# Kernel tuning notes

Measured on AMD Instinct MI355X. Metric: run time of the kernel, lower is better.

## Reference

```python
import jax, jax.numpy as jnp
import numpy as np

NS = 150  # MC weight samples


def setup_inputs() -> dict:
    key = jax.random.key(0)
    mu_shapes = {
        'mu_W0': (512, 784), 'mu_b0': (512,),
        'mu_W1': (512, 512), 'mu_b1': (512,),
        'mu_W2': (512, 512), 'mu_b2': (512,),
        'mu_W3': (10, 512),  'mu_b3': (10,),
    }
    ks = list(jax.random.split(key, 2 * len(mu_shapes) + 1))
    inp = {'x': jax.random.normal(ks[0], (64, 784), jnp.float32)}
    i = 1
    for name, shp in mu_shapes.items():
        inp[name] = jax.random.normal(ks[i], shp, jnp.float32) * 0.05
        i += 1
    for name, shp in mu_shapes.items():
        # log-std around -3 => std ~ 0.05
        inp['v_' + name[3:]] = jax.random.normal(ks[i], shp, jnp.float32) * 0.1 - 3.0
        i += 1
    return inp


def _sample(k, mu, v):
    # original: r = randn_like(m) * sqrt(exp(2*v)) == randn * exp(v); param = r + m
    eps = jax.random.normal(k, (NS,) + mu.shape, mu.dtype)
    return mu + jnp.exp(v) * eps  # [NS, *mu.shape]


def reference(x, mu_W0, mu_b0, mu_W1, mu_b1, mu_W2, mu_b2, mu_W3, mu_b3,
              v_W0, v_b0, v_W1, v_b1, v_W2, v_b2, v_W3, v_b3):
    ks = jax.random.split(jax.random.key(1), 8)
    W0 = _sample(ks[0], mu_W0, v_W0); b0 = _sample(ks[1], mu_b0, v_b0)
    W1 = _sample(ks[2], mu_W1, v_W1); b1 = _sample(ks[3], mu_b1, v_b1)
    W2 = _sample(ks[4], mu_W2, v_W2); b2 = _sample(ks[5], mu_b2, v_b2)
    W3 = _sample(ks[6], mu_W3, v_W3); b3 = _sample(ks[7], mu_b3, v_b3)
    # batched-over-samples MLP forward: s = sample, b = batch
    h = jax.nn.relu(jnp.einsum('bi,soi->sbo', x, W0) + b0[:, None, :])
    h = jax.nn.relu(jnp.einsum('sbi,soi->sbo', h, W1) + b1[:, None, :])
    h = jax.nn.relu(jnp.einsum('sbi,soi->sbo', h, W2) + b2[:, None, :])
    out = jnp.einsum('sbi,soi->sbo', h, W3) + b3[:, None, :]  # [NS, B, 10]
    return out
```

## Files before the change

kernel.cpp:

```cpp
#include <hip/hip_runtime.h>


typedef short bf16x8 __attribute__((ext_vector_type(8)));
typedef int   i32x4  __attribute__((ext_vector_type(4)));
typedef float f32x4  __attribute__((ext_vector_type(4)));

#define TF_R(r) { x0 += x1; x1 = (x1 << (r)) | (x1 >> (32 - (r))); x1 ^= x0; }

#define TF8(r) { _Pragma("unroll") for (int j = 0; j < 8; ++j) { \
    a[j] += b[j]; b[j] = (b[j] << (r)) | (b[j] >> (32 - (r))); b[j] ^= a[j]; } }
#define INJ8(kka, kkb) { _Pragma("unroll") for (int j = 0; j < 8; ++j) { \
    a[j] += (kka); b[j] += (kkb); } }

__device__ __forceinline__ unsigned int tf_xor(unsigned int k0, unsigned int k1,
                                               unsigned int c1)
{
  const unsigned int ks2 = k0 ^ k1 ^ 0x1BD11BDAu;
  unsigned int x0 = k0;
  unsigned int x1 = c1 + k1;
  TF_R(13) TF_R(15) TF_R(26) TF_R(6)
  x0 += k1;  x1 += ks2 + 1u;
  TF_R(17) TF_R(29) TF_R(16) TF_R(24)
  x0 += ks2; x1 += k0 + 2u;
  TF_R(13) TF_R(15) TF_R(26) TF_R(6)
  x0 += k0;  x1 += k1 + 3u;
  TF_R(17) TF_R(29) TF_R(16) TF_R(24)
  x0 += k1;  x1 += ks2 + 4u;
  TF_R(13) TF_R(15) TF_R(26) TF_R(6)
  x0 += ks2; x1 += k0 + 5u;
  return x0 ^ x1;
}

__device__ __forceinline__ float bits_to_g(unsigned int r)
{
  float f = __uint_as_float((r >> 9) | 0x3F800000u) - 1.0f;
  float x = __builtin_fmaf(f, 2.0f, -0.99999994f);
  float L = __log2f(__builtin_fmaf(-x, x, 1.0f));
  float t  = __builtin_fmaf(L, -0.6931472f, -2.5f);
  float pc = -4.39150654e-06f;
  pc = __builtin_fmaf(pc, t, 0.00021858087f);
  pc = __builtin_fmaf(pc, t, -0.00125372503f);
  pc = __builtin_fmaf(pc, t, -0.00417768164f);
  pc = __builtin_fmaf(pc, t, 0.246640727f);
  pc = __builtin_fmaf(pc, t, 1.50140941f);
  float w  = L * -0.6931472f;
  float t2 = sqrtf(w) - 3.0f;
  float pt = 0.00573950773f;
  pt = __builtin_fmaf(pt, t2, -0.0076224613f);
  pt = __builtin_fmaf(pt, t2, 0.00943887047f);
  pt = __builtin_fmaf(pt, t2, 1.00167406f);
  pt = __builtin_fmaf(pt, t2, 2.83297682f);
  float p = (L > -7.2134752f) ? pc : pt;
  return p * x;
}

__device__ __forceinline__ unsigned short f32_to_bf16_rne(float v)
{
  unsigned int u = __float_as_uint(v);
  unsigned int r = (u + 0x7FFFu + ((u >> 16) & 1u)) >> 16;
  return (unsigned short)r;
}

__device__ __forceinline__ unsigned int pack_bf16_rne(float a, float b)
{
  unsigned int ua = __float_as_uint(a);
  unsigned int ub = __float_as_uint(b);
  ua += 0x7FFFu + ((ua >> 16) & 1u);
  ub += 0x7FFFu + ((ub >> 16) & 1u);
  return __builtin_amdgcn_perm(ub, ua, 0x07060302u);
}

__global__ __launch_bounds__(256) void xpad_kernel(const float* __restrict__ x,
                                                   unsigned short* __restrict__ xp)
{
  int i = blockIdx.x * 256 + threadIdx.x;
  if (i >= 64 * 832) return;
  int m = i / 832, k = i - m * 832;
  float v = (k < 784) ? x[m * 784 + k] : 0.0f;
  xp[i] = f32_to_bf16_rne(v);
}

__global__ __launch_bounds__(256) void pack_kernel(
    const float* __restrict__ muW0, const float* __restrict__ vW0,
    const float* __restrict__ muW1, const float* __restrict__ vW1,
    const float* __restrict__ muW2, const float* __restrict__ vW2,
    const float* __restrict__ muW3, const float* __restrict__ vW3,
    float2* __restrict__ msP0, float2* __restrict__ msP1,
    float2* __restrict__ msP2, float2* __restrict__ msP3)
{
  int b = blockIdx.x, tid = threadIdx.x;
  const float* mu; const float* v; float2* o;
  int KV, NV, osh, base;
  if (b < 1664)      { mu = muW0; v = vW0; o = msP0; KV = 784; NV = 512; osh = 9; base = 0;    }
  else if (b < 2688) { mu = muW1; v = vW1; o = msP1; KV = 512; NV = 512; osh = 9; base = 1664; }
  else if (b < 3712) { mu = muW2; v = vW2; o = msP2; KV = 512; NV = 512; osh = 9; base = 2688; }
  else               { mu = muW3; v = vW3; o = msP3; KV = 512; NV = 10;  osh = 4; base = 3712; }
  int e = (b - base) * 256 + tid;
  int k = (e & 7) | ((e >> (3 + osh)) << 3);
  int n = (e >> 3) & ((1 << osh) - 1);
  float2 r = {0.0f, 0.0f};
  if (k < KV && n < NV) {
    r.x = mu[n * KV + k];
    r.y = __expf(v[n * KV + k]) * 1.41421356237f;
  }
  o[e] = r;
}

__global__ __launch_bounds__(256) void bias_kernel(
    const float* __restrict__ mu0, const float* __restrict__ v0, float* __restrict__ o0,
    const float* __restrict__ mu1, const float* __restrict__ v1, float* __restrict__ o1,
    const float* __restrict__ mu2, const float* __restrict__ v2, float* __restrict__ o2,
    const float* __restrict__ mu3, const float* __restrict__ v3, float* __restrict__ o3,
    unsigned int k00, unsigned int k01, unsigned int k10, unsigned int k11,
    unsigned int k20, unsigned int k21, unsigned int k30, unsigned int k31)
{
  int b = blockIdx.x, tid = threadIdx.x;
  int seg = b / 300; if (seg > 3) seg = 3;
  const float* mu; const float* v; float* o; unsigned int ka, kb; int n;
  if      (seg == 0) { mu = mu0; v = v0; o = o0; ka = k00; kb = k01; n = 76800; }
  else if (seg == 1) { mu = mu1; v = v1; o = o1; ka = k10; kb = k11; n = 76800; }
  else if (seg == 2) { mu = mu2; v = v2; o = o2; ka = k20; kb = k21; n = 76800; }
  else               { mu = mu3; v = v3; o = o3; ka = k30; kb = k31; n = 1500;  }
  int e = (b - seg * 300) * 256 + tid;
  if (e >= n) return;
  int oo = (seg == 3) ? (e % 10) : (e & 511);
  float eps = 1.41421356237f * bits_to_g(tf_xor(ka, kb, (unsigned int)e));
  o[e] = __builtin_fmaf(__expf(v[oo]), eps, mu[oo]);
}

template<int KVALID, int KPAD, int OVALID, int OPITCH, int ASTRIDE, int AROW,
         bool RELU, bool F32OUT>
__global__
__attribute__((amdgpu_flat_work_group_size(256, 256)))
__attribute__((amdgpu_waves_per_eu(1, 4)))
void layer_fused(
    const unsigned short* __restrict__ A,
    void* __restrict__ OutV,
    const float2* __restrict__ msP,
    const float* __restrict__ bS,
    unsigned int k0, unsigned int k1)
{
  constexpr int NSTEPS = KPAD / 32;
  const unsigned int ks2 = k0 ^ k1 ^ 0x1BD11BDAu;
  const int s    = blockIdx.y;
  const int tid  = threadIdx.x;
  const int wave = tid >> 6, lane = tid & 63;
  const int quad = lane >> 4;
  const int n16  = lane & 15;
  const int nlane = blockIdx.x * 16 + n16;

  const unsigned short* As = A + (size_t)s * ASTRIDE;
  const unsigned int idx_base = (unsigned int)s * (unsigned int)(OVALID * KVALID)
                              + (unsigned int)nlane * (unsigned int)KVALID;

  f32x4 acc[4] = {f32x4{0,0,0,0}, f32x4{0,0,0,0}, f32x4{0,0,0,0}, f32x4{0,0,0,0}};

  auto load_step = [&](int st, bf16x8 (&af)[4], float4 (&q)[4]) {
    const int kb = st * 32 + quad * 8;
    #pragma unroll
    for (int mt = 0; mt < 4; ++mt)
      af[mt] = *reinterpret_cast<const bf16x8*>(
          As + (size_t)(mt * 16 + n16) * AROW + kb);
    const float4* mp = reinterpret_cast<const float4*>(
        msP + ((size_t)(kb >> 3) * OPITCH + nlane) * 8);
    #pragma unroll
    for (int h = 0; h < 4; ++h)
      q[h] = mp[h];
  };

  auto compute_step = [&](int st, bf16x8 (&af)[4], float4 (&q)[4]) {
    const int kb = st * 32 + quad * 8;

    unsigned int a[8], b[8];
    const unsigned int cb = idx_base + (unsigned int)kb + k1;
    #pragma unroll
    for (int j = 0; j < 8; ++j) { a[j] = k0; b[j] = cb + (unsigned int)j; }
    TF8(13) TF8(15) TF8(26) TF8(6)  INJ8(k1, ks2 + 1u)
    TF8(17) TF8(29) TF8(16) TF8(24) INJ8(ks2, k0 + 2u)
    TF8(13) TF8(15) TF8(26) TF8(6)  INJ8(k0, k1 + 3u)
    TF8(17) TF8(29) TF8(16) TF8(24) INJ8(k1, ks2 + 4u)
    TF8(13) TF8(15) TF8(26) TF8(6)  INJ8(ks2, k0 + 5u)

    float g[8];
    #pragma unroll
    for (int j = 0; j < 8; ++j)
      g[j] = bits_to_g(a[j] ^ b[j]);

    float wv[8];
    wv[0] = __builtin_fmaf(q[0].y, g[0], q[0].x);
    wv[1] = __builtin_fmaf(q[0].w, g[1], q[0].z);
    wv[2] = __builtin_fmaf(q[1].y, g[2], q[1].x);
    wv[3] = __builtin_fmaf(q[1].w, g[3], q[1].z);
    wv[4] = __builtin_fmaf(q[2].y, g[4], q[2].x);
    wv[5] = __builtin_fmaf(q[2].w, g[5], q[2].z);
    wv[6] = __builtin_fmaf(q[3].y, g[6], q[3].x);
    wv[7] = __builtin_fmaf(q[3].w, g[7], q[3].z);

    i32x4 bp;
    #pragma unroll
    for (int h = 0; h < 4; ++h)
      bp[h] = (int)pack_bf16_rne(wv[2 * h], wv[2 * h + 1]);
    bf16x8 bfrag = __builtin_bit_cast(bf16x8, bp);

    #pragma unroll
    for (int mt = 0; mt < 4; ++mt)
      acc[mt] = __builtin_amdgcn_mfma_f32_16x16x32_bf16(af[mt], bfrag, acc[mt], 0, 0, 0);
  };

  bf16x8 afA[4], afB[4];
  float4 qA[4], qB[4];
  int st = wave;
  if (st < NSTEPS) load_step(st, afA, qA);
  while (st < NSTEPS) {
    int n1 = st + 4;
    if (n1 < NSTEPS) load_step(n1, afB, qB);
    __builtin_amdgcn_sched_barrier(0);
    compute_step(st, afA, qA);
    st = n1;
    if (st >= NSTEPS) break;
    int n2 = st + 4;
    if (n2 < NSTEPS) load_step(n2, afA, qA);
    __builtin_amdgcn_sched_barrier(0);
    compute_step(st, afB, qB);
    st = n2;
  }

  __shared__ float red[4 * 16 * 64];
  #pragma unroll
  for (int mt = 0; mt < 4; ++mt)
    #pragma unroll
    for (int r = 0; r < 4; ++r)
      red[(wave * 16 + mt * 4 + r) * 64 + lane] = acc[mt][r];
  __syncthreads();

  const int m   = tid >> 2;
  const int nq  = (tid & 3) * 4;
  const int row = (m >> 4) * 4 + (m & 3);
  const int col = ((m >> 2) & 3) * 16 + nq;

  float4 p0 = *reinterpret_cast<const float4*>(&red[(0 * 16 + row) * 64 + col]);
  float4 p1 = *reinterpret_cast<const float4*>(&red[(1 * 16 + row) * 64 + col]);
  float4 p2 = *reinterpret_cast<const float4*>(&red[(2 * 16 + row) * 64 + col]);
  float4 p3 = *reinterpret_cast<const float4*>(&red[(3 * 16 + row) * 64 + col]);
  float v0 = (p0.x + p1.x) + (p2.x + p3.x);
  float v1 = (p0.y + p1.y) + (p2.y + p3.y);
  float v2 = (p0.z + p1.z) + (p2.z + p3.z);
  float v3 = (p0.w + p1.w) + (p2.w + p3.w);

  if (F32OUT) {
    float* Out = (float*)OutV;
    float vv[4] = {v0, v1, v2, v3};
    #pragma unroll
    for (int jj = 0; jj < 4; ++jj) {
      int nn = nq + jj;
      if (nn < OVALID)
        Out[((size_t)s * 64 + m) * OVALID + nn] = vv[jj] + bS[s * OVALID + nn];
    }
  } else {
    const float4 b4 = *reinterpret_cast<const float4*>(
        &bS[s * OVALID + blockIdx.x * 16 + nq]);
    float o0 = v0 + b4.x, o1 = v1 + b4.y, o2 = v2 + b4.z, o3 = v3 + b4.w;
    if (RELU) {
      o0 = fmaxf(o0, 0.0f); o1 = fmaxf(o1, 0.0f);
      o2 = fmaxf(o2, 0.0f); o3 = fmaxf(o3, 0.0f);
    }
    uint2 stv;
    stv.x = pack_bf16_rne(o0, o1);
    stv.y = pack_bf16_rne(o2, o3);
    *reinterpret_cast<uint2*>(
        (unsigned short*)OutV + ((size_t)s * 64 + m) * OPITCH + blockIdx.x * 16 + nq) = stv;
  }
}

static void tf_host(unsigned int k0, unsigned int k1, unsigned int c0, unsigned int c1,
                    unsigned int* o0, unsigned int* o1)
{
  const unsigned int ks2 = k0 ^ k1 ^ 0x1BD11BDAu;
  unsigned int x0 = c0 + k0, x1 = c1 + k1;
  TF_R(13) TF_R(15) TF_R(26) TF_R(6)
  x0 += k1;  x1 += ks2 + 1u;
  TF_R(17) TF_R(29) TF_R(16) TF_R(24)
  x0 += ks2; x1 += k0 + 2u;
  TF_R(13) TF_R(15) TF_R(26) TF_R(6)
  x0 += k0;  x1 += k1 + 3u;
  TF_R(17) TF_R(29) TF_R(16) TF_R(24)
  x0 += k1;  x1 += ks2 + 4u;
  TF_R(13) TF_R(15) TF_R(26) TF_R(6)
  x0 += ks2; x1 += k0 + 5u;
  *o0 = x0; *o1 = x1;
}

extern "C" void kernel_launch(void* const* d_in, const int* in_sizes, int n_in,
                              void* d_out, int out_size, void* d_ws, size_t ws_size,
                              hipStream_t stream)
{
  (void)in_sizes; (void)n_in; (void)out_size; (void)ws_size;

  const float* x    = (const float*)d_in[0];
  const float* muW0 = (const float*)d_in[1];
  const float* mub0 = (const float*)d_in[2];
  const float* muW1 = (const float*)d_in[3];
  const float* mub1 = (const float*)d_in[4];
  const float* muW2 = (const float*)d_in[5];
  const float* mub2 = (const float*)d_in[6];
  const float* muW3 = (const float*)d_in[7];
  const float* mub3 = (const float*)d_in[8];
  const float* vW0  = (const float*)d_in[9];
  const float* vb0  = (const float*)d_in[10];
  const float* vW1  = (const float*)d_in[11];
  const float* vb1  = (const float*)d_in[12];
  const float* vW2  = (const float*)d_in[13];
  const float* vb2  = (const float*)d_in[14];
  const float* vW3  = (const float*)d_in[15];
  const float* vb3  = (const float*)d_in[16];

  unsigned int key[8][2];
  for (unsigned int i = 0; i < 8; ++i)
    tf_host(0u, 1u, 0u, i, &key[i][0], &key[i][1]);

  char* ws = (char*)d_ws;
  unsigned short* xp = (unsigned short*)(ws);
  unsigned short* hA = (unsigned short*)(ws + 106496);
  float* b0s  = (float*)(ws + 9936896);
  float* b1s  = (float*)(ws + 10244096);
  float* b2s  = (float*)(ws + 10551296);
  float* b3s  = (float*)(ws + 10858496);
  float2* msP1 = (float2*)(ws + 10866688);
  float2* msP2 = (float2*)(ws + 12963840);
  float2* msP3 = (float2*)(ws + 15060992);
  float2* msP0 = (float2*)(ws + 15126528);
  unsigned short* hB = (unsigned short*)(ws + 15126528);

  xpad_kernel<<<208, 256, 0, stream>>>(x, xp);
  pack_kernel<<<3744, 256, 0, stream>>>(muW0, vW0, muW1, vW1, muW2, vW2, muW3, vW3,
                                        msP0, msP1, msP2, msP3);
  bias_kernel<<<906, 256, 0, stream>>>(mub0, vb0, b0s, mub1, vb1, b1s,
                                       mub2, vb2, b2s, mub3, vb3, b3s,
                                       key[1][0], key[1][1], key[3][0], key[3][1],
                                       key[5][0], key[5][1], key[7][0], key[7][1]);

  layer_fused<784, 832, 512, 512, 0,     832, true,  false>
      <<<dim3(32, 150), 256, 0, stream>>>(xp, hA, msP0, b0s, key[0][0], key[0][1]);
  layer_fused<512, 512, 512, 512, 32768, 512, true,  false>
      <<<dim3(32, 150), 256, 0, stream>>>(hA, hB, msP1, b1s, key[2][0], key[2][1]);
  layer_fused<512, 512, 512, 512, 32768, 512, true,  false>
      <<<dim3(32, 150), 256, 0, stream>>>(hB, hA, msP2, b2s, key[4][0], key[4][1]);
  layer_fused<512, 512, 10,  16,  32768, 512, false, true>
      <<<dim3(1, 150), 256, 0, stream>>>(hA, d_out, msP3, b3s, key[6][0], key[6][1]);
}
```

Baseline: 453.8 us.

## Split fused weight-sampling GEMM into separate weight-generation and GEMM kernels

```diff
diff --git a/kernel.cpp b/kernel.cpp
--- a/kernel.cpp
+++ b/kernel.cpp
@@ -128,6 +128,133 @@
   o[e] = __builtin_fmaf(__expf(v[oo]), eps, mu[oo]);
 }
 
+template<int KVALID, int KPAD>
+__global__ __launch_bounds__(256) void genw_kernel(
+    unsigned short* __restrict__ W,
+    const float2* __restrict__ msP,
+    unsigned int k0, unsigned int k1)
+{
+  constexpr int CPR = KPAD / 32;
+  const unsigned int ks2 = k0 ^ k1 ^ 0x1BD11BDAu;
+  const int e = blockIdx.x * 256 + threadIdx.x;
+  const int s = blockIdx.y;
+  const int n = e / CPR;
+  const int c32 = e - n * CPR;
+  const int k32 = c32 * 32;
+
+  const unsigned int cb0 = (unsigned int)s * (unsigned int)(512 * KVALID)
+                         + (unsigned int)n * (unsigned int)KVALID
+                         + (unsigned int)k32;
+  unsigned short* wp = W + ((size_t)(s * 512 + n) * KPAD + k32);
+
+  #pragma unroll
+  for (int h = 0; h < 4; ++h) {
+    const int kb = k32 + h * 8;
+    const float4* mp = reinterpret_cast<const float4*>(
+        msP + ((size_t)(kb >> 3) * 512 + n) * 8);
+    float4 q0 = mp[0], q1 = mp[1], q2 = mp[2], q3 = mp[3];
+
+    unsigned int a[8], b[8];
+    const unsigned int cb = cb0 + (unsigned int)(h * 8) + k1;
+    #pragma unroll
+    for (int j = 0; j < 8; ++j) { a[j] = k0; b[j] = cb + (unsigned int)j; }
+    TF8(13) TF8(15) TF8(26) TF8(6)  INJ8(k1, ks2 + 1u)
+    TF8(17) TF8(29) TF8(16) TF8(24) INJ8(ks2, k0 + 2u)
+    TF8(13) TF8(15) TF8(26) TF8(6)  INJ8(k0, k1 + 3u)
+    TF8(17) TF8(29) TF8(16) TF8(24) INJ8(k1, ks2 + 4u)
+    TF8(13) TF8(15) TF8(26) TF8(6)  INJ8(ks2, k0 + 5u)
+
+    float g[8];
+    #pragma unroll
+    for (int j = 0; j < 8; ++j)
+      g[j] = bits_to_g(a[j] ^ b[j]);
+
+    float wv[8];
+    wv[0] = __builtin_fmaf(q0.y, g[0], q0.x);
+    wv[1] = __builtin_fmaf(q0.w, g[1], q0.z);
+    wv[2] = __builtin_fmaf(q1.y, g[2], q1.x);
+    wv[3] = __builtin_fmaf(q1.w, g[3], q1.z);
+    wv[4] = __builtin_fmaf(q2.y, g[4], q2.x);
+    wv[5] = __builtin_fmaf(q2.w, g[5], q2.z);
+    wv[6] = __builtin_fmaf(q3.y, g[6], q3.x);
+    wv[7] = __builtin_fmaf(q3.w, g[7], q3.z);
+
+    i32x4 bp;
+    #pragma unroll
+    for (int hh = 0; hh < 4; ++hh)
+      bp[hh] = (int)pack_bf16_rne(wv[2 * hh], wv[2 * hh + 1]);
+    *reinterpret_cast<i32x4*>(wp + h * 8) = bp;
+  }
+}
+
+template<int KPAD, int ASTRIDE, int AROW>
+__global__ __launch_bounds__(256) void gemm_kernel(
+    const unsigned short* __restrict__ A,
+    unsigned short* __restrict__ Out,
+    const unsigned short* __restrict__ W,
+    const float* __restrict__ bS,
+    int unused0, int unused1)
+{
+  constexpr int NSTEPS = KPAD / 32;
+  const int s    = blockIdx.y;
+  const int tid  = threadIdx.x;
+  const int wave = tid >> 6, lane = tid & 63;
+  const int quad = lane >> 4;
+  const int n16  = lane & 15;
+  const int nlane = blockIdx.x * 16 + n16;
+
+  const unsigned short* As = A + (size_t)s * ASTRIDE;
+  const unsigned short* Wr = W + (size_t)(s * 512 + nlane) * KPAD;
+
+  f32x4 acc[4] = {f32x4{0,0,0,0}, f32x4{0,0,0,0}, f32x4{0,0,0,0}, f32x4{0,0,0,0}};
+
+  #pragma unroll 1
+  for (int st = wave; st < NSTEPS; st += 4) {
+    const int kb = st * 32 + quad * 8;
+    bf16x8 afrag[4];
+    #pragma unroll
+    for (int mt = 0; mt < 4; ++mt)
+      afrag[mt] = *reinterpret_cast<const bf16x8*>(
+          As + (size_t)(mt * 16 + n16) * AROW + kb);
+    bf16x8 bfrag = *reinterpret_cast<const bf16x8*>(Wr + kb);
+    #pragma unroll
+    for (int mt = 0; mt < 4; ++mt)
+      acc[mt] = __builtin_amdgcn_mfma_f32_16x16x32_bf16(afrag[mt], bfrag, acc[mt], 0, 0, 0);
+  }
+
+  __shared__ float red[4 * 16 * 64];
+  #pragma unroll
+  for (int mt = 0; mt < 4; ++mt)
+    #pragma unroll
+    for (int r = 0; r < 4; ++r)
+      red[(wave * 16 + mt * 4 + r) * 64 + lane] = acc[mt][r];
+  __syncthreads();
+
+  const int m   = tid >> 2;
+  const int nq  = (tid & 3) * 4;
+  const int row = (m >> 4) * 4 + (m & 3);
+  const int col = ((m >> 2) & 3) * 16 + nq;
+
+  float4 p0 = *reinterpret_cast<const float4*>(&red[(0 * 16 + row) * 64 + col]);
+  float4 p1 = *reinterpret_cast<const float4*>(&red[(1 * 16 + row) * 64 + col]);
+  float4 p2 = *reinterpret_cast<const float4*>(&red[(2 * 16 + row) * 64 + col]);
+  float4 p3 = *reinterpret_cast<const float4*>(&red[(3 * 16 + row) * 64 + col]);
+  float v0 = (p0.x + p1.x) + (p2.x + p3.x);
+  float v1 = (p0.y + p1.y) + (p2.y + p3.y);
+  float v2 = (p0.z + p1.z) + (p2.z + p3.z);
+  float v3 = (p0.w + p1.w) + (p2.w + p3.w);
+
+  const float4 b4 = *reinterpret_cast<const float4*>(
+      &bS[s * 512 + blockIdx.x * 16 + nq]);
+  float o0 = fmaxf(v0 + b4.x, 0.0f), o1 = fmaxf(v1 + b4.y, 0.0f);
+  float o2 = fmaxf(v2 + b4.z, 0.0f), o3 = fmaxf(v3 + b4.w, 0.0f);
+  uint2 stv;
+  stv.x = pack_bf16_rne(o0, o1);
+  stv.y = pack_bf16_rne(o2, o3);
+  *reinterpret_cast<uint2*>(
+      Out + ((size_t)s * 64 + m) * 512 + blockIdx.x * 16 + nq) = stv;
+}
+
 template<int KVALID, int KPAD, int OVALID, int OPITCH, int ASTRIDE, int AROW,
          bool RELU, bool F32OUT>
 __global__
@@ -170,7 +297,6 @@
 
   auto compute_step = [&](int st, bf16x8 (&af)[4], float4 (&q)[4]) {
     const int kb = st * 32 + quad * 8;
-
     unsigned int a[8], b[8];
     const unsigned int cb = idx_base + (unsigned int)kb + k1;
     #pragma unroll
@@ -294,7 +420,7 @@
                               void* d_out, int out_size, void* d_ws, size_t ws_size,
                               hipStream_t stream)
 {
-  (void)in_sizes; (void)n_in; (void)out_size; (void)ws_size;
+  (void)in_sizes; (void)n_in; (void)out_size;
 
   const float* x    = (const float*)d_in[0];
   const float* muW0 = (const float*)d_in[1];
@@ -330,6 +456,10 @@
   float2* msP3 = (float2*)(ws + 15060992);
   float2* msP0 = (float2*)(ws + 15126528);
   unsigned short* hB = (unsigned short*)(ws + 15126528);
+  unsigned short* Wbuf = (unsigned short*)(ws + 25165824);
+
+  const bool splitMid = ws_size >= (size_t)25165824 + 78643200u;
+  const bool splitL0  = ws_size >= (size_t)25165824 + 127795200u;
 
   xpad_kernel<<<208, 256, 0, stream>>>(x, xp);
   pack_kernel<<<3744, 256, 0, stream>>>(muW0, vW0, muW1, vW1, muW2, vW2, muW3, vW3,
@@ -339,12 +469,32 @@
                                        key[1][0], key[1][1], key[3][0], key[3][1],
                                        key[5][0], key[5][1], key[7][0], key[7][1]);
 
-  layer_fused<784, 832, 512, 512, 0,     832, true,  false>
-      <<<dim3(32, 150), 256, 0, stream>>>(xp, hA, msP0, b0s, key[0][0], key[0][1]);
-  layer_fused<512, 512, 512, 512, 32768, 512, true,  false>
-      <<<dim3(32, 150), 256, 0, stream>>>(hA, hB, msP1, b1s, key[2][0], key[2][1]);
-  layer_fused<512, 512, 512, 512, 32768, 512, true,  false>
-      <<<dim3(32, 150), 256, 0, stream>>>(hB, hA, msP2, b2s, key[4][0], key[4][1]);
-  layer_fused<512, 512, 10,  16,  32768, 512, false, true>
+  if (splitL0) {
+    genw_kernel<784, 832><<<dim3(52, 150), 256, 0, stream>>>(
+        Wbuf, msP0, key[0][0], key[0][1]);
+    gemm_kernel<832, 0, 832><<<dim3(32, 150), 256, 0, stream>>>(
+        xp, hA, Wbuf, b0s, 0, 0);
+  } else {
+    layer_fused<784, 832, 512, 512, 0, 832, true, false>
+        <<<dim3(32, 150), 256, 0, stream>>>(xp, hA, msP0, b0s, key[0][0], key[0][1]);
+  }
+
+  if (splitMid) {
+    genw_kernel<512, 512><<<dim3(32, 150), 256, 0, stream>>>(
+        Wbuf, msP1, key[2][0], key[2][1]);
+    gemm_kernel<512, 32768, 512><<<dim3(32, 150), 256, 0, stream>>>(
+        hA, hB, Wbuf, b1s, 0, 0);
+    genw_kernel<512, 512><<<dim3(32, 150), 256, 0, stream>>>(
+        Wbuf, msP2, key[4][0], key[4][1]);
+    gemm_kernel<512, 32768, 512><<<dim3(32, 150), 256, 0, stream>>>(
+        hB, hA, Wbuf, b2s, 0, 0);
+  } else {
+    layer_fused<512, 512, 512, 512, 32768, 512, true, false>
+        <<<dim3(32, 150), 256, 0, stream>>>(hA, hB, msP1, b1s, key[2][0], key[2][1]);
+    layer_fused<512, 512, 512, 512, 32768, 512, true, false>
+        <<<dim3(32, 150), 256, 0, stream>>>(hB, hA, msP2, b2s, key[4][0], key[4][1]);
+  }
+
+  layer_fused<512, 512, 10, 16, 32768, 512, false, true>
       <<<dim3(1, 150), 256, 0, stream>>>(hA, d_out, msP3, b3s, key[6][0], key[6][1]);
 }
```

Result: slower. 609.2 us (+34.2%).

## Split final layer across K with atomic accumulation and bias-prefilled output

Applied to the files above, without the earlier changes.

```diff
diff --git a/kernel.cpp b/kernel.cpp
--- a/kernel.cpp
+++ b/kernel.cpp
@@ -128,19 +128,30 @@
   o[e] = __builtin_fmaf(__expf(v[oo]), eps, mu[oo]);
 }
 
-template<int KVALID, int KPAD, int OVALID, int OPITCH, int ASTRIDE, int AROW,
-         bool RELU, bool F32OUT>
+__global__ __launch_bounds__(256) void bias3_out(float* __restrict__ Out,
+                                                 const float* __restrict__ b3s)
+{
+  int i = blockIdx.x * 256 + threadIdx.x;
+  if (i >= 96000) return;
+  int s = i / 640;
+  int rem = i - s * 640;
+  int n = rem % 10;
+  Out[i] = b3s[s * 10 + n];
+}
+
+template<int KVALID, int KPAD, int ASTRIDE, int AROW>
 __global__
 __attribute__((amdgpu_flat_work_group_size(256, 256)))
 __attribute__((amdgpu_waves_per_eu(1, 4)))
 void layer_fused(
     const unsigned short* __restrict__ A,
-    void* __restrict__ OutV,
+    unsigned short* __restrict__ Out,
     const float2* __restrict__ msP,
     const float* __restrict__ bS,
     unsigned int k0, unsigned int k1)
 {
   constexpr int NSTEPS = KPAD / 32;
+  constexpr int OVALID = 512, OPITCH = 512;
   const unsigned int ks2 = k0 ^ k1 ^ 0x1BD11BDAu;
   const int s    = blockIdx.y;
   const int tid  = threadIdx.x;
@@ -170,7 +181,6 @@
 
   auto compute_step = [&](int st, bf16x8 (&af)[4], float4 (&q)[4]) {
     const int kb = st * 32 + quad * 8;
-
     unsigned int a[8], b[8];
     const unsigned int cb = idx_base + (unsigned int)kb + k1;
     #pragma unroll
@@ -247,28 +257,106 @@
   float v2 = (p0.z + p1.z) + (p2.z + p3.z);
   float v3 = (p0.w + p1.w) + (p2.w + p3.w);
 
-  if (F32OUT) {
-    float* Out = (float*)OutV;
-    float vv[4] = {v0, v1, v2, v3};
-    #pragma unroll
-    for (int jj = 0; jj < 4; ++jj) {
-      int nn = nq + jj;
-      if (nn < OVALID)
-        Out[((size_t)s * 64 + m) * OVALID + nn] = vv[jj] + bS[s * OVALID + nn];
-    }
-  } else {
-    const float4 b4 = *reinterpret_cast<const float4*>(
-        &bS[s * OVALID + blockIdx.x * 16 + nq]);
-    float o0 = v0 + b4.x, o1 = v1 + b4.y, o2 = v2 + b4.z, o3 = v3 + b4.w;
-    if (RELU) {
-      o0 = fmaxf(o0, 0.0f); o1 = fmaxf(o1, 0.0f);
-      o2 = fmaxf(o2, 0.0f); o3 = fmaxf(o3, 0.0f);
-    }
-    uint2 stv;
-    stv.x = pack_bf16_rne(o0, o1);
-    stv.y = pack_bf16_rne(o2, o3);
-    *reinterpret_cast<uint2*>(
-        (unsigned short*)OutV + ((size_t)s * 64 + m) * OPITCH + blockIdx.x * 16 + nq) = stv;
+  const float4 b4 = *reinterpret_cast<const float4*>(
+      &bS[s * OVALID + blockIdx.x * 16 + nq]);
+  float o0 = fmaxf(v0 + b4.x, 0.0f), o1 = fmaxf(v1 + b4.y, 0.0f);
+  float o2 = fmaxf(v2 + b4.z, 0.0f), o3 = fmaxf(v3 + b4.w, 0.0f);
+  uint2 stv;
+  stv.x = pack_bf16_rne(o0, o1);
+  stv.y = pack_bf16_rne(o2, o3);
+  *reinterpret_cast<uint2*>(
+      Out + ((size_t)s * 64 + m) * OPITCH + blockIdx.x * 16 + nq) = stv;
+}
+
+__global__ __launch_bounds__(256) void layer3_atomic(
+    const unsigned short* __restrict__ A,
+    float* __restrict__ Out,
+    const float2* __restrict__ msP,
+    unsigned int k0, unsigned int k1)
+{
+  const unsigned int ks2 = k0 ^ k1 ^ 0x1BD11BDAu;
+  const int s    = blockIdx.y;
+  const int tid  = threadIdx.x;
+  const int wave = tid >> 6, lane = tid & 63;
+  const int quad = lane >> 4;
+  const int n    = lane & 15;
+
+  const unsigned short* As = A + (size_t)s * (64 * 512);
+  const int st = blockIdx.x * 4 + wave;
+  const int kb = st * 32 + quad * 8;
+  const unsigned int idx_base = (unsigned int)s * 5120u + (unsigned int)n * 512u;
+
+  const float4* mp = reinterpret_cast<const float4*>(
+      msP + ((size_t)(kb >> 3) * 16 + n) * 8);
+  float4 q0 = mp[0], q1 = mp[1], q2 = mp[2], q3 = mp[3];
+
+  unsigned int a[8], b[8];
+  const unsigned int cb = idx_base + (unsigned int)kb + k1;
+  #pragma unroll
+  for (int j = 0; j < 8; ++j) { a[j] = k0; b[j] = cb + (unsigned int)j; }
+  TF8(13) TF8(15) TF8(26) TF8(6)  INJ8(k1, ks2 + 1u)
+  TF8(17) TF8(29) TF8(16) TF8(24) INJ8(ks2, k0 + 2u)
+  TF8(13) TF8(15) TF8(26) TF8(6)  INJ8(k0, k1 + 3u)
+  TF8(17) TF8(29) TF8(16) TF8(24) INJ8(k1, ks2 + 4u)
+  TF8(13) TF8(15) TF8(26) TF8(6)  INJ8(ks2, k0 + 5u)
+
+  float g[8];
+  #pragma unroll
+  for (int j = 0; j < 8; ++j)
+    g[j] = bits_to_g(a[j] ^ b[j]);
+
+  float wv[8];
+  wv[0] = __builtin_fmaf(q0.y, g[0], q0.x);
+  wv[1] = __builtin_fmaf(q0.w, g[1], q0.z);
+  wv[2] = __builtin_fmaf(q1.y, g[2], q1.x);
+  wv[3] = __builtin_fmaf(q1.w, g[3], q1.z);
+  wv[4] = __builtin_fmaf(q2.y, g[4], q2.x);
+  wv[5] = __builtin_fmaf(q2.w, g[5], q2.z);
+  wv[6] = __builtin_fmaf(q3.y, g[6], q3.x);
+  wv[7] = __builtin_fmaf(q3.w, g[7], q3.z);
+
+  i32x4 bp;
+  #pragma unroll
+  for (int h = 0; h < 4; ++h)
+    bp[h] = (int)pack_bf16_rne(wv[2 * h], wv[2 * h + 1]);
+  bf16x8 bfrag = __builtin_bit_cast(bf16x8, bp);
+
+  f32x4 acc[4] = {f32x4{0,0,0,0}, f32x4{0,0,0,0}, f32x4{0,0,0,0}, f32x4{0,0,0,0}};
+  #pragma unroll
+  for (int mt = 0; mt < 4; ++mt) {
+    bf16x8 afrag = *reinterpret_cast<const bf16x8*>(
+        As + (size_t)(mt * 16 + n) * 512 + kb);
+    acc[mt] = __builtin_amdgcn_mfma_f32_16x16x32_bf16(afrag, bfrag, acc[mt], 0, 0, 0);
+  }
+
+  __shared__ float red[4 * 16 * 64];
+  #pragma unroll
+  for (int mt = 0; mt < 4; ++mt)
+    #pragma unroll
+    for (int r = 0; r < 4; ++r)
+      red[(wave * 16 + mt * 4 + r) * 64 + lane] = acc[mt][r];
+  __syncthreads();
+
+  const int m   = tid >> 2;
+  const int nq  = (tid & 3) * 4;
+  const int row = (m >> 4) * 4 + (m & 3);
+  const int col = ((m >> 2) & 3) * 16 + nq;
+
+  float4 p0 = *reinterpret_cast<const float4*>(&red[(0 * 16 + row) * 64 + col]);
+  float4 p1 = *reinterpret_cast<const float4*>(&red[(1 * 16 + row) * 64 + col]);
+  float4 p2 = *reinterpret_cast<const float4*>(&red[(2 * 16 + row) * 64 + col]);
+  float4 p3 = *reinterpret_cast<const float4*>(&red[(3 * 16 + row) * 64 + col]);
+  float vv[4];
+  vv[0] = (p0.x + p1.x) + (p2.x + p3.x);
+  vv[1] = (p0.y + p1.y) + (p2.y + p3.y);
+  vv[2] = (p0.z + p1.z) + (p2.z + p3.z);
+  vv[3] = (p0.w + p1.w) + (p2.w + p3.w);
+
+  #pragma unroll
+  for (int jj = 0; jj < 4; ++jj) {
+    int nn = nq + jj;
+    if (nn < 10)
+      atomicAdd(&Out[((size_t)s * 64 + m) * 10 + nn], vv[jj]);
   }
 }
 
@@ -338,13 +426,14 @@
                                        mub2, vb2, b2s, mub3, vb3, b3s,
                                        key[1][0], key[1][1], key[3][0], key[3][1],
                                        key[5][0], key[5][1], key[7][0], key[7][1]);
-
-  layer_fused<784, 832, 512, 512, 0,     832, true,  false>
-      <<<dim3(32, 150), 256, 0, stream>>>(xp, hA, msP0, b0s, key[0][0], key[0][1]);
-  layer_fused<512, 512, 512, 512, 32768, 512, true,  false>
-      <<<dim3(32, 150), 256, 0, stream>>>(hA, hB, msP1, b1s, key[2][0], key[2][1]);
-  layer_fused<512, 512, 512, 512, 32768, 512, true,  false>
-      <<<dim3(32, 150), 256, 0, stream>>>(hB, hA, msP2, b2s, key[4][0], key[4][1]);
-  layer_fused<512, 512, 10,  16,  32768, 512, false, true>
-      <<<dim3(1, 150), 256, 0, stream>>>(hA, d_out, msP3, b3s, key[6][0], key[6][1]);
-}
+  bias3_out<<<375, 256, 0, stream>>>((float*)d_out, b3s);
+
+  layer_fused<784, 832, 0,     832><<<dim3(32, 150), 256, 0, stream>>>(
+      xp, hA, msP0, b0s, key[0][0], key[0][1]);
+  layer_fused<512, 512, 32768, 512><<<dim3(32, 150), 256, 0, stream>>>(
+      hA, hB, msP1, b1s, key[2][0], key[2][1]);
+  layer_fused<512, 512, 32768, 512><<<dim3(32, 150), 256, 0, stream>>>(
+      hB, hA, msP2, b2s, key[4][0], key[4][1]);
+  layer3_atomic<<<dim3(4, 150), 256, 0, stream>>>(
+      hA, (float*)d_out, msP3, key[6][0], key[6][1]);
+}
```

Measured after the change: 454.0 us. No clear change (+0.1%).
